# Optimization experiments

Hardware: AMD Instinct MI355X
Metric: run time of the kernel (lower is better)

Reference implementation:

```python
import jax, jax.numpy as jnp
import numpy as np

S = 4096          # num tokens
H = 2304          # hidden_size
NQ = 8            # num query heads
NKV = 4           # num kv heads
HD = 256          # head_dim
INTER = 9216      # intermediate_size
SOFTCAP = 50.0    # attn_logit_softcapping
WINDOW = 1024     # sliding window
EPS = 1e-6
THETA = 10000.0
SCALE = 256.0 ** -0.5  # query_pre_attn_scalar ** -0.5


def rmsnorm(x, w, eps=EPS):
    # GemmaRMSNorm: x / rms(x) * (1 + w)
    var = jnp.mean(x * x, axis=-1, keepdims=True)
    return x * jax.lax.rsqrt(var + eps) * (1.0 + w)


def apply_rope(x, positions):
    # x: [S, nh, HD], neox style (rotate halves)
    half = HD // 2
    inv_freq = 1.0 / (THETA ** (jnp.arange(0, half, dtype=jnp.float32) / half))
    freqs = positions.astype(jnp.float32)[:, None] * inv_freq[None, :]  # [S, half]
    cos = jnp.cos(freqs)[:, None, :]
    sin = jnp.sin(freqs)[:, None, :]
    x1, x2 = x[..., :half], x[..., half:]
    return jnp.concatenate([x1 * cos - x2 * sin, x2 * cos + x1 * sin], axis=-1)


def setup_inputs() -> dict:
    key = jax.random.key(0)
    ks = jax.random.split(key, 6)
    w_std = 0.02
    return {
        "positions": jnp.arange(S, dtype=jnp.int32),
        "hidden_states": jax.random.normal(ks[0], (S, H), dtype=jnp.float32),
        "w_qkv": jax.random.normal(ks[1], (H, (NQ + 2 * NKV) * HD), dtype=jnp.float32) * w_std,
        "w_o": jax.random.normal(ks[2], (NQ * HD, H), dtype=jnp.float32) * w_std,
        "w_gate_up": jax.random.normal(ks[3], (H, 2 * INTER), dtype=jnp.float32) * w_std,
        "w_down": jax.random.normal(ks[4], (INTER, H), dtype=jnp.float32) * w_std,
        "w_in_ln": jnp.zeros((H,), jnp.float32),
        "w_post_attn_ln": jnp.zeros((H,), jnp.float32),
        "w_pre_ff_ln": jnp.zeros((H,), jnp.float32),
        "w_post_ff_ln": jnp.zeros((H,), jnp.float32),
    }


def attention(positions, h, w_qkv, w_o):
    qkv = h @ w_qkv  # [S, (NQ+2*NKV)*HD]
    q, k, v = jnp.split(qkv, [NQ * HD, (NQ + NKV) * HD], axis=-1)
    q = q.reshape(S, NQ, HD)
    k = k.reshape(S, NKV, HD)
    v = v.reshape(S, NKV, HD)
    q = apply_rope(q, positions)
    k = apply_rope(k, positions)
    # GQA: repeat kv heads
    rep = NQ // NKV
    k = jnp.repeat(k, rep, axis=1)  # [S, NQ, HD]
    v = jnp.repeat(v, rep, axis=1)
    scores = jnp.einsum("qhd,khd->hqk", q, k) * SCALE  # [NQ, S, S]
    # Gemma2 logit soft-capping
    scores = SOFTCAP * jnp.tanh(scores / SOFTCAP)
    # causal + sliding window mask
    i = jnp.arange(S)[:, None]
    j = jnp.arange(S)[None, :]
    ok = (j <= i) & (i - j < WINDOW)
    scores = jnp.where(ok[None], scores, -jnp.inf)
    probs = jax.nn.softmax(scores, axis=-1)
    out = jnp.einsum("hqk,khd->qhd", probs, v).reshape(S, NQ * HD)
    return out @ w_o


def mlp(x, w_gate_up, w_down):
    gu = x @ w_gate_up  # [S, 2*INTER]
    gate, up = jnp.split(gu, 2, axis=-1)
    return (jax.nn.gelu(gate, approximate=True) * up) @ w_down


def reference(positions, hidden_states, w_qkv, w_o, w_gate_up, w_down,
              w_in_ln, w_post_attn_ln, w_pre_ff_ln, w_post_ff_ln):
    # residual is None on entry (first layer semantics)
    residual = hidden_states
    h = rmsnorm(hidden_states, w_in_ln)
    h = attention(positions, h, w_qkv, w_o)
    h = rmsnorm(h, w_post_attn_ln)
    # fused add + norm: residual <- h + residual ; h <- norm(residual)
    residual = h + residual
    h = rmsnorm(residual, w_pre_ff_ln)
    h = mlp(h, w_gate_up, w_down)
    h = rmsnorm(h, w_post_ff_ln)
    return (h, residual)
```

## Files before the change

kernel.cpp:

```cpp
#include <hip/hip_runtime.h>
#include <cstdint>
#include <cmath>

#define S_LEN 4096
#define H_DIM 2304
#define NQH   8
#define NKVH  4
#define HDIM  256
#define INTER 9216
#define QKV_N 4096
#define QH    2048
#define KVH   1024

typedef __attribute__((ext_vector_type(4))) float  f32x4;
typedef __attribute__((ext_vector_type(8))) __bf16 bf16x8;

__device__ __forceinline__ __bf16 f2bf(float f) {
  union { float f; unsigned u; } x; x.f = f;
  unsigned r = (x.u + 0x7fffu + ((x.u >> 16) & 1u)) >> 16;
  union { unsigned short s; __bf16 b; } y; y.s = (unsigned short)r;
  return y.b;
}

__device__ __forceinline__ void g2l16(const void* g, void* l) {
  __builtin_amdgcn_global_load_lds(
      (__attribute__((address_space(1))) void*)(uintptr_t)g,
      (__attribute__((address_space(3))) void*)(uint32_t)(uintptr_t)l, 16, 0, 0);
}

__device__ __forceinline__ float block_sum(float v, float* sbuf) {
  #pragma unroll
  for (int o = 32; o > 0; o >>= 1) v += __shfl_xor(v, o);
  __syncthreads();
  if ((threadIdx.x & 63) == 0) sbuf[threadIdx.x >> 6] = v;
  __syncthreads();
  return sbuf[0] + sbuf[1] + sbuf[2] + sbuf[3];
}

__global__ void conv_t_kernel(const float* __restrict__ src, __bf16* __restrict__ dst,
                              int srcStride, int dstStride) {
  __shared__ float t[32][33];
  int tx = threadIdx.x & 31, ty = threadIdx.x >> 5;
  int n0 = blockIdx.x * 32, k0 = blockIdx.y * 32;
  #pragma unroll
  for (int l = 0; l < 4; ++l) {
    int ky = ty + l * 8;
    t[tx][ky] = src[(long)(k0 + ky) * srcStride + n0 + tx];
  }
  __syncthreads();
  #pragma unroll
  for (int l = 0; l < 4; ++l) {
    int ny = ty + l * 8;
    dst[(long)(n0 + ny) * dstStride + k0 + tx] = f2bf(t[ny][tx]);
  }
}

__device__ __forceinline__ int gu_map(int n) {
  int t = n >> 7, w = (n >> 6) & 1, j = (n >> 4) & 3, c = n & 15;
  int a = t * 64 + w * 32 + ((j >> 1) << 4) + c;
  return (j & 1) ? (INTER + a) : a;
}

__global__ void conv_gu_kernel(const float* __restrict__ src, __bf16* __restrict__ dst) {
  __shared__ float t[32][33];
  int tx = threadIdx.x & 31, ty = threadIdx.x >> 5;
  int n0 = blockIdx.x * 32, k0 = blockIdx.y * 32;
  int sc = gu_map(n0 + tx);
  #pragma unroll
  for (int l = 0; l < 4; ++l) {
    int ky = ty + l * 8;
    t[tx][ky] = src[(long)(k0 + ky) * (2 * INTER) + sc];
  }
  __syncthreads();
  #pragma unroll
  for (int l = 0; l < 4; ++l) {
    int ny = ty + l * 8;
    dst[(long)(n0 + ny) * H_DIM + k0 + tx] = f2bf(t[ny][tx]);
  }
}

__global__ void rms_in_kernel(const float* __restrict__ x, const float* __restrict__ w,
                              __bf16* __restrict__ out) {
  __shared__ float sbuf[4];
  int row = blockIdx.x, tid = threadIdx.x;
  const float* xr = x + (long)row * H_DIM;
  float v[9]; float ss = 0.f;
  #pragma unroll
  for (int i = 0; i < 9; ++i) { v[i] = xr[tid + i * 256]; ss += v[i] * v[i]; }
  ss = block_sum(ss, sbuf);
  float inv = rsqrtf(ss * (1.0f / H_DIM) + 1e-6f);
  #pragma unroll
  for (int i = 0; i < 9; ++i)
    out[(long)row * H_DIM + tid + i * 256] = f2bf(v[i] * inv * (1.f + w[tid + i * 256]));
}

__global__ void rms_post_attn_kernel(const float* __restrict__ P, const float* __restrict__ hidden,
                                     const float* __restrict__ w_post, const float* __restrict__ w_pre,
                                     float* __restrict__ resid, __bf16* __restrict__ x2) {
  __shared__ float sbuf[4];
  int row = blockIdx.x, tid = threadIdx.x;
  const float* pr = P + (long)row * H_DIM;
  const float* hr = hidden + (long)row * H_DIM;
  float pv[9]; float ss = 0.f;
  #pragma unroll
  for (int i = 0; i < 9; ++i) { pv[i] = pr[tid + i * 256]; ss += pv[i] * pv[i]; }
  ss = block_sum(ss, sbuf);
  float inv = rsqrtf(ss * (1.0f / H_DIM) + 1e-6f);
  float rv[9]; float ss2 = 0.f;
  #pragma unroll
  for (int i = 0; i < 9; ++i) {
    int c = tid + i * 256;
    float hn = pv[i] * inv * (1.f + w_post[c]);
    rv[i] = hn + hr[c];
    resid[(long)row * H_DIM + c] = rv[i];
    ss2 += rv[i] * rv[i];
  }
  ss2 = block_sum(ss2, sbuf);
  float inv2 = rsqrtf(ss2 * (1.0f / H_DIM) + 1e-6f);
  #pragma unroll
  for (int i = 0; i < 9; ++i) {
    int c = tid + i * 256;
    x2[(long)row * H_DIM + c] = f2bf(rv[i] * inv2 * (1.f + w_pre[c]));
  }
}

__global__ void rms_final_kernel(const float* __restrict__ x, const float* __restrict__ w,
                                 float* __restrict__ out) {
  __shared__ float sbuf[4];
  int row = blockIdx.x, tid = threadIdx.x;
  const float* xr = x + (long)row * H_DIM;
  float v[9]; float ss = 0.f;
  #pragma unroll
  for (int i = 0; i < 9; ++i) { v[i] = xr[tid + i * 256]; ss += v[i] * v[i]; }
  ss = block_sum(ss, sbuf);
  float inv = rsqrtf(ss * (1.0f / H_DIM) + 1e-6f);
  #pragma unroll
  for (int i = 0; i < 9; ++i)
    out[(long)row * H_DIM + tid + i * 256] = v[i] * inv * (1.f + w[tid + i * 256]);
}

__global__ void rope_kernel(const float* __restrict__ qkv, const int* __restrict__ positions,
                            __bf16* __restrict__ Qr, __bf16* __restrict__ Kr) {
  int row = blockIdx.x, tid = threadIdx.x;
  float pos = (float)positions[row];
  const float* src = qkv + (long)row * QKV_N;
  const float LOG_TH_128 = 9.210340371976184f / 128.f;
  #pragma unroll
  for (int l = 0; l < 4; ++l) {
    int p = tid + l * 256;
    int hh = p >> 7, d = p & 127;
    float fr = pos * expf(-(float)d * LOG_TH_128);
    float sn, cs; sincosf(fr, &sn, &cs);
    float x1 = src[hh * 256 + d], x2 = src[hh * 256 + d + 128];
    Qr[(long)row * QH + hh * 256 + d]       = f2bf(x1 * cs - x2 * sn);
    Qr[(long)row * QH + hh * 256 + d + 128] = f2bf(x2 * cs + x1 * sn);
  }
  #pragma unroll
  for (int l = 0; l < 2; ++l) {
    int p = tid + l * 256;
    int hh = p >> 7, d = p & 127;
    float fr = pos * expf(-(float)d * LOG_TH_128);
    float sn, cs; sincosf(fr, &sn, &cs);
    float x1 = src[QH + hh * 256 + d], x2 = src[QH + hh * 256 + d + 128];
    Kr[(long)row * KVH + hh * 256 + d]       = f2bf(x1 * cs - x2 * sn);
    Kr[(long)row * KVH + hh * 256 + d + 128] = f2bf(x2 * cs + x1 * sn);
  }
}

template <int EPI>
__global__ void gemm_bt(const __bf16* __restrict__ A, const __bf16* __restrict__ B,
                        void* __restrict__ Cout, int K, int ldc) {
  __shared__ __bf16 As[128 * 64];
  __shared__ __bf16 Bs[128 * 64];
  int tid = threadIdx.x;
  int wave = tid >> 6, lane = tid & 63;
  int wm = wave >> 1, wn = wave & 1;
  int q4 = lane >> 4, l15 = lane & 15;
  long bm = (long)blockIdx.y * 128, bn = (long)blockIdx.x * 128;

  int r8 = tid >> 3;
  int cs = (tid & 7) ^ (r8 & 7);
  const __bf16* Ag = A + (bm + r8) * K + cs * 8;
  const __bf16* Bg = B + (bn + r8) * K + cs * 8;
  __bf16* Asd = As + tid * 8;
  __bf16* Bsd = Bs + tid * 8;

  int moff[4], noff[4];
  #pragma unroll
  for (int i = 0; i < 4; ++i) {
    moff[i] = (wm * 64 + i * 16 + l15) * 64;
    noff[i] = (wn * 64 + i * 16 + l15) * 64;
  }
  int c0 = (q4 ^ (l15 & 7)) * 8;
  f32x4 acc[4][4] = {};

  for (int k0 = 0; k0 < K; k0 += 64) {
    #pragma unroll
    for (int l = 0; l < 4; ++l) {
      g2l16(Ag + (long)(l * 32) * K, Asd + l * 2048);
      g2l16(Bg + (long)(l * 32) * K, Bsd + l * 2048);
    }
    Ag += 64; Bg += 64;
    __syncthreads();
    #pragma unroll
    for (int ks = 0; ks < 2; ++ks) {
      int cc = c0 ^ (ks * 32);
      bf16x8 af[4], bfv[4];
      #pragma unroll
      for (int i = 0; i < 4; ++i) af[i]  = *(const bf16x8*)(As + moff[i] + cc);
      #pragma unroll
      for (int j = 0; j < 4; ++j) bfv[j] = *(const bf16x8*)(Bs + noff[j] + cc);
      #pragma unroll
      for (int i = 0; i < 4; ++i)
        #pragma unroll
        for (int j = 0; j < 4; ++j)
          acc[i][j] = __builtin_amdgcn_mfma_f32_16x16x32_bf16(af[i], bfv[j], acc[i][j], 0, 0, 0);
    }
    __syncthreads();
  }

  if (EPI == 0) {
    float* C = (float*)Cout;
    #pragma unroll
    for (int i = 0; i < 4; ++i)
      #pragma unroll
      for (int r = 0; r < 4; ++r) {
        long m = bm + wm * 64 + i * 16 + q4 * 4 + r;
        #pragma unroll
        for (int j = 0; j < 4; ++j)
          C[m * ldc + bn + wn * 64 + j * 16 + l15] = acc[i][j][r];
      }
  } else {
    __bf16* C = (__bf16*)Cout;
    #pragma unroll
    for (int i = 0; i < 4; ++i)
      #pragma unroll
      for (int r = 0; r < 4; ++r) {
        long m = bm + wm * 64 + i * 16 + q4 * 4 + r;
        #pragma unroll
        for (int jj = 0; jj < 2; ++jj) {
          float gt = acc[i][2 * jj][r];
          float up = acc[i][2 * jj + 1][r];
          float u = 0.7978845608f * (gt + 0.044715f * gt * gt * gt);
          float e = __builtin_amdgcn_exp2f(u * 2.8853900817779268f);
          float gl = gt * (1.0f - __builtin_amdgcn_rcpf(e + 1.0f));
          long a = (bn >> 1) + wn * 32 + jj * 16 + l15;
          C[m * ldc + a] = f2bf(gl * up);
        }
      }
  }
}

__global__ void attn_kernel(const __bf16* __restrict__ Qr, const __bf16* __restrict__ Kr,
                            const __bf16* __restrict__ VT, __bf16* __restrict__ AT) {
  __shared__ __bf16 Kt[64 * 256];
  __shared__ __bf16 Vt[256 * 64];
  __shared__ __bf16 Pt[4][16 * 72];
  int tid = threadIdx.x, wave = tid >> 6, lane = tid & 63;
  int q4 = lane >> 4, l15 = lane & 15;
  int h = blockIdx.y, hk = h >> 1;
  int qb = blockIdx.x * 64;
  int wqb = qb + wave * 16;

  bf16x8 qf[8];
  {
    const __bf16* qp = Qr + (long)(wqb + l15) * QH + h * HDIM + q4 * 8;
    #pragma unroll
    for (int ks = 0; ks < 8; ++ks) qf[ks] = *(const bf16x8*)(qp + ks * 32);
  }
  f32x4 Oa[16] = {};
  float lsum[4] = {0.f, 0.f, 0.f, 0.f};

  int csk = (tid & 31) ^ ((tid >> 5) & 7);
  const __bf16* Kh = Kr + (long)(tid >> 5) * KVH + hk * HDIM + csk * 8;
  int csv = (tid & 7) ^ ((tid >> 3) & 7);
  const __bf16* Vh = VT + (long)(hk * HDIM + (tid >> 3)) * S_LEN + csv * 8;

  int lo = qb - 1023; if (lo < 0) lo = 0;
  int t0 = lo >> 6, t1 = qb >> 6;
  for (int t = t0; t <= t1; ++t) {
    int k0 = t * 64;
    #pragma unroll
    for (int l = 0; l < 8; ++l) {
      g2l16(Kh + ((long)k0 + l * 8) * KVH, Kt + tid * 8 + l * 2048);
      g2l16(Vh + k0 + (long)(l * 32) * S_LEN, Vt + tid * 8 + l * 2048);
    }
    __syncthreads();
    bool active = (k0 <= wqb + 15) && (k0 + 63 >= wqb - 1023);
    if (active) {
      f32x4 Sa[4] = {};
      #pragma unroll
      for (int ks = 0; ks < 8; ++ks)
        #pragma unroll
        for (int j = 0; j < 4; ++j) {
          int key = j * 16 + l15;
          int cc = (ks * 4 + q4) ^ (l15 & 7);
          bf16x8 kf = *(const bf16x8*)(Kt + key * 256 + cc * 8);
          Sa[j] = __builtin_amdgcn_mfma_f32_16x16x32_bf16(qf[ks], kf, Sa[j], 0, 0, 0);
        }
      #pragma unroll
      for (int r = 0; r < 4; ++r) {
        int qi = wqb + q4 * 4 + r;
        #pragma unroll
        for (int j = 0; j < 4; ++j) {
          int kj = k0 + j * 16 + l15;
          float y = Sa[j][r] * 1.25e-3f;
          float e = __builtin_amdgcn_exp2f(y * 2.8853900817779268f);
          float p = __builtin_amdgcn_exp2f(72.13475204444817f
                     - 144.26950408889634f * __builtin_amdgcn_rcpf(e + 1.0f));
          bool ok = (kj <= qi) && (qi - kj < 1024);
          p = ok ? p : 0.0f;
          lsum[r] += p;
          Pt[wave][(q4 * 4 + r) * 72 + j * 16 + l15] = f2bf(p);
        }
      }
      asm volatile("s_waitcnt lgkmcnt(0)" ::: "memory");
      bf16x8 pf[2];
      #pragma unroll
      for (int ks = 0; ks < 2; ++ks)
        pf[ks] = *(const bf16x8*)(&Pt[wave][l15 * 72 + ks * 32 + q4 * 8]);
      #pragma unroll
      for (int f = 0; f < 16; ++f) {
        int d = f * 16 + l15;
        #pragma unroll
        for (int ks = 0; ks < 2; ++ks) {
          int cc = (ks * 4 + q4) ^ (l15 & 7);
          bf16x8 vf = *(const bf16x8*)(Vt + d * 64 + cc * 8);
          Oa[f] = __builtin_amdgcn_mfma_f32_16x16x32_bf16(pf[ks], vf, Oa[f], 0, 0, 0);
        }
      }
    }
    __syncthreads();
  }
  #pragma unroll
  for (int r = 0; r < 4; ++r) {
    float v = lsum[r];
    #pragma unroll
    for (int o = 1; o < 16; o <<= 1) v += __shfl_xor(v, o);
    lsum[r] = __builtin_amdgcn_rcpf(v);
  }
  #pragma unroll
  for (int f = 0; f < 16; ++f)
    #pragma unroll
    for (int r = 0; r < 4; ++r) {
      long qi = wqb + q4 * 4 + r;
      AT[qi * QH + h * HDIM + f * 16 + l15] = f2bf(Oa[f][r] * lsum[r]);
    }
}

extern "C" void kernel_launch(void* const* d_in, const int* in_sizes, int n_in,
                              void* d_out, int out_size, void* d_ws, size_t ws_size,
                              hipStream_t stream) {
  (void)in_sizes; (void)n_in; (void)out_size; (void)ws_size;
  const int*   positions = (const int*)d_in[0];
  const float* hidden    = (const float*)d_in[1];
  const float* w_qkv     = (const float*)d_in[2];
  const float* w_o       = (const float*)d_in[3];
  const float* w_gu      = (const float*)d_in[4];
  const float* w_dn      = (const float*)d_in[5];
  const float* w_in_ln   = (const float*)d_in[6];
  const float* w_post    = (const float*)d_in[7];
  const float* w_pre     = (const float*)d_in[8];
  const float* w_pff     = (const float*)d_in[9];
  float* out_h   = (float*)d_out;
  float* out_res = out_h + (size_t)S_LEN * H_DIM;

  char* p = (char*)d_ws;
  auto take = [&](size_t b) { char* r = p; p += (b + 255) & ~(size_t)255; return r; };
  __bf16* Wqkv = (__bf16*)take((size_t)QKV_N * H_DIM * 2);
  __bf16* Wo   = (__bf16*)take((size_t)H_DIM * QH * 2);
  __bf16* Wgu  = (__bf16*)take((size_t)2 * INTER * H_DIM * 2);
  __bf16* Wdn  = (__bf16*)take((size_t)H_DIM * INTER * 2);
  __bf16* Xn   = (__bf16*)take((size_t)S_LEN * H_DIM * 2);
  char*   Rbig = take((size_t)S_LEN * INTER * 2);
  __bf16* Qrb  = (__bf16*)take((size_t)S_LEN * QH * 2);
  __bf16* Krb  = (__bf16*)take((size_t)S_LEN * KVH * 2);
  __bf16* VTb  = (__bf16*)take((size_t)KVH * S_LEN * 2);
  __bf16* ATb  = (__bf16*)take((size_t)S_LEN * QH * 2);
  float*  Pf   = (float*)take((size_t)S_LEN * H_DIM * 4);
  __bf16* X2   = (__bf16*)take((size_t)S_LEN * H_DIM * 2);
  float*  QKV  = (float*)Rbig;
  __bf16* ACT  = (__bf16*)Rbig;
  float*  Mbuf = Pf;

  dim3 blk(256);
  conv_t_kernel<<<dim3(QKV_N / 32, H_DIM / 32), blk, 0, stream>>>(w_qkv, Wqkv, QKV_N, H_DIM);
  conv_t_kernel<<<dim3(H_DIM / 32, QH / 32),    blk, 0, stream>>>(w_o,   Wo,   H_DIM, QH);
  conv_gu_kernel<<<dim3(2 * INTER / 32, H_DIM / 32), blk, 0, stream>>>(w_gu, Wgu);
  conv_t_kernel<<<dim3(H_DIM / 32, INTER / 32), blk, 0, stream>>>(w_dn,  Wdn,  H_DIM, INTER);
  rms_in_kernel<<<S_LEN, blk, 0, stream>>>(hidden, w_in_ln, Xn);
  gemm_bt<0><<<dim3(QKV_N / 128, S_LEN / 128), blk, 0, stream>>>(Xn, Wqkv, QKV, H_DIM, QKV_N);
  rope_kernel<<<S_LEN, blk, 0, stream>>>(QKV, positions, Qrb, Krb);
  conv_t_kernel<<<dim3(KVH / 32, S_LEN / 32), blk, 0, stream>>>(QKV + QH + KVH, VTb, QKV_N, S_LEN);
  attn_kernel<<<dim3(S_LEN / 64, NQH), blk, 0, stream>>>(Qrb, Krb, VTb, ATb);
  gemm_bt<0><<<dim3(H_DIM / 128, S_LEN / 128), blk, 0, stream>>>(ATb, Wo, Pf, QH, H_DIM);
  rms_post_attn_kernel<<<S_LEN, blk, 0, stream>>>(Pf, hidden, w_post, w_pre, out_res, X2);
  gemm_bt<1><<<dim3(2 * INTER / 128, S_LEN / 128), blk, 0, stream>>>(X2, Wgu, ACT, H_DIM, INTER);
  gemm_bt<0><<<dim3(H_DIM / 128, S_LEN / 128), blk, 0, stream>>>(ACT, Wdn, Mbuf, INTER, H_DIM);
  rms_final_kernel<<<S_LEN, blk, 0, stream>>>(Mbuf, w_pff, out_h);
}
```

Measured before the change: 1.278 ms.

## Add 256x256-tile 8-wave GEMM with phased LDS pipeline for QKV and gate-up

Adds a new GEMM kernel that uses 256x256 output tiles with 512 threads, double-buffered swizzled LDS, an interleaved load/MFMA phase schedule with explicit waitcnt and setprio, and XCD-aware block remapping. It is used for the QKV projection and the fused gate-up+GELU GEMM. The larger tiles raise arithmetic intensity and cut global traffic, but they use more LDS and registers per workgroup. The QKV grid is also small (16x16 blocks), which may leave some CUs underused.

```diff
diff --git a/kernel.cpp b/kernel.cpp
--- a/kernel.cpp
+++ b/kernel.cpp
@@ -248,6 +248,164 @@
           C[m * ldc + a] = f2bf(gl * up);
         }
       }
+  }
+}
+
+template <int EPI>
+__global__ __launch_bounds__(512, 2)
+void gemm8(const __bf16* __restrict__ A, const __bf16* __restrict__ B,
+           void* __restrict__ Cout, int K, int ldc) {
+  __shared__ __bf16 As[2][16384];
+  __shared__ __bf16 Bs[2][16384];
+  const __bf16* Asb = (const __bf16*)As;
+  const __bf16* Bsb = (const __bf16*)Bs;
+
+  int tid = threadIdx.x;
+  int wave = tid >> 6, lane = tid & 63;
+  int wm = wave >> 2;
+  int wn = wave & 3;
+  int q4 = lane >> 4, l15 = lane & 15;
+  int xk = l15 & 7;
+
+  int nwgx = gridDim.x;
+  int nwg = nwgx * gridDim.y;
+  int orig = blockIdx.y * nwgx + blockIdx.x;
+  int qd = nwg >> 3, rm = nwg & 7;
+  int xcd = orig & 7, idx = orig >> 3;
+  int swz = (xcd < rm ? xcd * (qd + 1) : rm * (qd + 1) + (xcd - rm) * qd) + idx;
+  long bm = (long)(swz / nwgx) * 256;
+  long bn = (long)(swz % nwgx) * 256;
+
+  int rr = tid >> 3;
+  int cs = (tid & 7) ^ (rr & 7);
+  const __bf16* Ag = A + (bm + rr) * (long)K + cs * 8;
+  const __bf16* Bg = B + (bn + rr) * (long)K + cs * 8;
+  __bf16* Asd = (__bf16*)As + tid * 8;
+  __bf16* Bsd = (__bf16*)Bs + tid * 8;
+
+#define ST_A(buf, h, kof) do { \
+    g2l16(Ag + ((h) * 128LL      ) * K + (kof), Asd + (buf) * 16384 + (h) * 8192); \
+    g2l16(Ag + ((h) * 128LL + 64 ) * K + (kof), Asd + (buf) * 16384 + (h) * 8192 + 4096); } while (0)
+#define ST_B(buf, h, kof) do { \
+    g2l16(Bg + ((h) * 128LL      ) * K + (kof), Bsd + (buf) * 16384 + (h) * 8192); \
+    g2l16(Bg + ((h) * 128LL + 64 ) * K + (kof), Bsd + (buf) * 16384 + (h) * 8192 + 4096); } while (0)
+
+  int aOff[4], bOff[4];
+  #pragma unroll
+  for (int i = 0; i < 4; ++i) {
+    aOff[i] = (wm * 64 + i * 16 + l15) * 64;
+    bOff[i] = (wn * 64 + i * 16 + l15) * 64;
+  }
+
+#define PH_LOAD_A(buf, mh, ks) \
+  { _Pragma("unroll") for (int f = 0; f < 4; ++f) \
+      afr[f] = *(const bf16x8*)(Asb + (buf) * 16384 + (mh) * 8192 + aOff[f] + ((((ks) * 4 + q4) ^ xk) * 8)); }
+#define PH_LOAD_B(buf) \
+  { _Pragma("unroll") for (int ks2 = 0; ks2 < 2; ++ks2) \
+    _Pragma("unroll") for (int j = 0; j < 4; ++j) \
+      bfr[ks2][j] = *(const bf16x8*)(Bsb + (buf) * 16384 + bOff[j] + (((ks2 * 4 + q4) ^ xk) * 8)); }
+#define PH_CORE(mh, ks) \
+  __builtin_amdgcn_s_barrier(); \
+  asm volatile("s_waitcnt lgkmcnt(0)" ::: "memory"); \
+  __builtin_amdgcn_s_setprio(1); \
+  { _Pragma("unroll") for (int f = 0; f < 4; ++f) \
+    _Pragma("unroll") for (int j = 0; j < 4; ++j) \
+      acc[(mh) * 4 + f][j] = __builtin_amdgcn_mfma_f32_16x16x32_bf16(afr[f], bfr[ks][j], acc[(mh) * 4 + f][j], 0, 0, 0); } \
+  __builtin_amdgcn_s_setprio(0)
+#define BAR   __builtin_amdgcn_s_barrier()
+#define WVM6  asm volatile("s_waitcnt vmcnt(6)" ::: "memory")
+#define WVM0  asm volatile("s_waitcnt vmcnt(0)" ::: "memory")
+
+  f32x4 acc[8][4] = {};
+  bf16x8 bfr[2][4];
+  bf16x8 afr[4];
+
+  int nt = K >> 6;
+  int nit = (nt >> 1) - 1;
+
+  ST_B(0, 0, 0); ST_B(0, 1, 0); ST_A(0, 0, 0); ST_A(0, 1, 0);
+  ST_B(1, 0, 64); ST_B(1, 1, 64); ST_A(1, 0, 64);
+  WVM6;
+  BAR;
+
+  for (int it = 0; it < nit; ++it) {
+    const long k0 = (long)it * 128;
+    PH_LOAD_B(0); PH_LOAD_A(0, 0, 0); ST_A(1, 1, k0 + 64);
+    asm volatile("s_waitcnt lgkmcnt(8)" ::: "memory");
+    PH_CORE(0, 0); BAR;
+    PH_LOAD_A(0, 0, 1); ST_B(0, 0, k0 + 128);
+    PH_CORE(0, 1); BAR;
+    PH_LOAD_A(0, 1, 0); ST_B(0, 1, k0 + 128);
+    PH_CORE(1, 0); BAR;
+    PH_LOAD_A(0, 1, 1); ST_A(0, 0, k0 + 128);
+    PH_CORE(1, 1); WVM6; BAR;
+    PH_LOAD_B(1); PH_LOAD_A(1, 0, 0); ST_A(0, 1, k0 + 128);
+    asm volatile("s_waitcnt lgkmcnt(8)" ::: "memory");
+    PH_CORE(0, 0); BAR;
+    PH_LOAD_A(1, 0, 1); ST_B(1, 0, k0 + 192);
+    PH_CORE(0, 1); BAR;
+    PH_LOAD_A(1, 1, 0); ST_B(1, 1, k0 + 192);
+    PH_CORE(1, 0); BAR;
+    PH_LOAD_A(1, 1, 1); ST_A(1, 0, k0 + 192);
+    PH_CORE(1, 1); WVM6; BAR;
+  }
+
+  {
+    const long k0 = (long)(nt - 2) * 64;
+    PH_LOAD_B(0); PH_LOAD_A(0, 0, 0); ST_A(1, 1, k0 + 64);
+    asm volatile("s_waitcnt lgkmcnt(8)" ::: "memory");
+    PH_CORE(0, 0); BAR;
+    PH_LOAD_A(0, 0, 1); PH_CORE(0, 1); BAR;
+    PH_LOAD_A(0, 1, 0); PH_CORE(1, 0); BAR;
+    PH_LOAD_A(0, 1, 1); PH_CORE(1, 1); WVM0; BAR;
+    PH_LOAD_B(1); PH_LOAD_A(1, 0, 0); PH_CORE(0, 0); BAR;
+    PH_LOAD_A(1, 0, 1); PH_CORE(0, 1); BAR;
+    PH_LOAD_A(1, 1, 0); PH_CORE(1, 0); BAR;
+    PH_LOAD_A(1, 1, 1); PH_CORE(1, 1);
+  }
+
+#undef ST_A
+#undef ST_B
+#undef PH_LOAD_A
+#undef PH_LOAD_B
+#undef PH_CORE
+#undef BAR
+#undef WVM6
+#undef WVM0
+
+  if (EPI == 0) {
+    float* C = (float*)Cout;
+    #pragma unroll
+    for (int mi = 0; mi < 8; ++mi) {
+      int mh = mi >> 2, f = mi & 3;
+      #pragma unroll
+      for (int r = 0; r < 4; ++r) {
+        long m = bm + mh * 128 + wm * 64 + f * 16 + q4 * 4 + r;
+        #pragma unroll
+        for (int j = 0; j < 4; ++j)
+          C[m * ldc + bn + wn * 64 + j * 16 + l15] = acc[mi][j][r];
+      }
+    }
+  } else {
+    __bf16* C = (__bf16*)Cout;
+    #pragma unroll
+    for (int mi = 0; mi < 8; ++mi) {
+      int mh = mi >> 2, f = mi & 3;
+      #pragma unroll
+      for (int r = 0; r < 4; ++r) {
+        long m = bm + mh * 128 + wm * 64 + f * 16 + q4 * 4 + r;
+        #pragma unroll
+        for (int jj = 0; jj < 2; ++jj) {
+          float gt = acc[mi][2 * jj][r];
+          float up = acc[mi][2 * jj + 1][r];
+          float u = 0.7978845608f * (gt + 0.044715f * gt * gt * gt);
+          float e = __builtin_amdgcn_exp2f(u * 2.8853900817779268f);
+          float gl = gt * (1.0f - __builtin_amdgcn_rcpf(e + 1.0f));
+          long a = (bn >> 1) + (wn >> 1) * 64 + (wn & 1) * 32 + jj * 16 + l15;
+          C[m * ldc + a] = f2bf(gl * up);
+        }
+      }
+    }
   }
 }
 
@@ -389,13 +547,13 @@
   conv_gu_kernel<<<dim3(2 * INTER / 32, H_DIM / 32), blk, 0, stream>>>(w_gu, Wgu);
   conv_t_kernel<<<dim3(H_DIM / 32, INTER / 32), blk, 0, stream>>>(w_dn,  Wdn,  H_DIM, INTER);
   rms_in_kernel<<<S_LEN, blk, 0, stream>>>(hidden, w_in_ln, Xn);
-  gemm_bt<0><<<dim3(QKV_N / 128, S_LEN / 128), blk, 0, stream>>>(Xn, Wqkv, QKV, H_DIM, QKV_N);
+  gemm8<0><<<dim3(QKV_N / 256, S_LEN / 256), dim3(512), 0, stream>>>(Xn, Wqkv, QKV, H_DIM, QKV_N);
   rope_kernel<<<S_LEN, blk, 0, stream>>>(QKV, positions, Qrb, Krb);
   conv_t_kernel<<<dim3(KVH / 32, S_LEN / 32), blk, 0, stream>>>(QKV + QH + KVH, VTb, QKV_N, S_LEN);
   attn_kernel<<<dim3(S_LEN / 64, NQH), blk, 0, stream>>>(Qrb, Krb, VTb, ATb);
   gemm_bt<0><<<dim3(H_DIM / 128, S_LEN / 128), blk, 0, stream>>>(ATb, Wo, Pf, QH, H_DIM);
   rms_post_attn_kernel<<<S_LEN, blk, 0, stream>>>(Pf, hidden, w_post, w_pre, out_res, X2);
-  gemm_bt<1><<<dim3(2 * INTER / 128, S_LEN / 128), blk, 0, stream>>>(X2, Wgu, ACT, H_DIM, INTER);
+  gemm8<1><<<dim3(2 * INTER / 256, S_LEN / 256), dim3(512), 0, stream>>>(X2, Wgu, ACT, H_DIM, INTER);
   gemm_bt<0><<<dim3(H_DIM / 128, S_LEN / 128), blk, 0, stream>>>(ACT, Wdn, Mbuf, INTER, H_DIM);
   rms_final_kernel<<<S_LEN, blk, 0, stream>>>(Mbuf, w_pff, out_h);
 }
```

Result: faster. 1.233 ms (-3.5%).
